# Kernel optimization log

Hardware: AMD Instinct MI355X
Metric: run time of the kernel (lower is better)

Reference implementation:

```python
import jax, jax.numpy as jnp
import numpy as np

N = 200_000   # nodes per type
F_IN = 64     # input features per node type
H = 8         # hidden_channels (heads=1)
E = 3_000_000 # edges per edge type


def setup_inputs() -> dict:
    key = jax.random.key(0)
    ks = jax.random.split(key, 40)
    d = {}
    d['x_ind'] = jax.random.normal(ks[0], (N, F_IN), jnp.float32)
    d['x_org'] = jax.random.normal(ks[1], (N, F_IN), jnp.float32)
    d['x_ext'] = jax.random.normal(ks[2], (N, F_IN), jnp.float32)
    d['ei_ind_org'] = jax.random.randint(ks[3], (2, E), 0, N, jnp.int32)
    d['ei_org_ind'] = jax.random.randint(ks[4], (2, E), 0, N, jnp.int32)
    d['ei_ext_ind'] = jax.random.randint(ks[5], (2, E), 0, N, jnp.int32)
    d['ei_ext_org'] = jax.random.randint(ks[6], (2, E), 0, N, jnp.int32)
    s_in = 1.0 / np.sqrt(F_IN)
    # per-node-type projections (Linear(F_IN, H) with bias)
    for i, nt in enumerate(('ind', 'org', 'ext')):
        d[f'W_{nt}'] = jax.random.normal(ks[7 + i], (F_IN, H), jnp.float32) * s_in
        d[f'b_{nt}'] = jnp.zeros((H,), jnp.float32)
    # per-edge-type GAT attention vectors (heads=1, so shape [H])
    for i, et in enumerate(('ind_org', 'org_ind', 'ext_ind', 'ext_org')):
        d[f'att_src_{et}'] = jax.random.normal(ks[10 + 2 * i], (H,), jnp.float32) * (1.0 / np.sqrt(H))
        d[f'att_dst_{et}'] = jax.random.normal(ks[11 + 2 * i], (H,), jnp.float32) * (1.0 / np.sqrt(H))
    # semantic attention: k_lin(H->H) + query q
    d['k_W'] = jax.random.normal(ks[20], (H, H), jnp.float32) * (1.0 / np.sqrt(H))
    d['k_b'] = jnp.zeros((H,), jnp.float32)
    d['q'] = jax.random.normal(ks[21], (H,), jnp.float32)
    # prediction heads
    d['lin_ind_W'] = jax.random.normal(ks[22], (H, 1), jnp.float32) * (1.0 / np.sqrt(H))
    d['lin_ind_b'] = jnp.zeros((1,), jnp.float32)
    d['lin_org_W'] = jax.random.normal(ks[23], (H, 1), jnp.float32) * (1.0 / np.sqrt(H))
    d['lin_org_b'] = jnp.zeros((1,), jnp.float32)
    return d


def _gat_edge(h_src, h_dst, a_src, a_dst, ei):
    """Per-edge-type GAT message passing with segment softmax over dst."""
    row, col = ei[0], ei[1]
    alpha_s = h_src @ a_src  # [N]
    alpha_d = h_dst @ a_dst  # [N]
    alpha = jax.nn.leaky_relu(alpha_s[row] + alpha_d[col], 0.2)  # [E]
    m = jax.lax.stop_gradient(jax.ops.segment_max(alpha, col, num_segments=N))
    m = jnp.where(jnp.isfinite(m), m, 0.0)
    ex = jnp.exp(alpha - m[col])
    den = jax.ops.segment_sum(ex, col, num_segments=N) + 1e-16
    w = ex / den[col]  # [E]
    out = jax.ops.segment_sum(h_src[row] * w[:, None], col, num_segments=N)  # [N,H]
    return jax.nn.relu(out)


def _group(outs, q, k_W, k_b):
    """Semantic-level attention over metapath embeddings."""
    o = jnp.stack(outs)  # [M, N, H]
    score = (jnp.tanh(o @ k_W + k_b) @ q).mean(axis=1)  # [M]
    attn = jax.nn.softmax(score)
    return jnp.einsum('m,mnf->nf', attn, o)


def reference(x_ind, x_org, x_ext,
              ei_ind_org, ei_org_ind, ei_ext_ind, ei_ext_org,
              W_ind, b_ind, W_org, b_org, W_ext, b_ext,
              att_src_ind_org, att_dst_ind_org,
              att_src_org_ind, att_dst_org_ind,
              att_src_ext_ind, att_dst_ext_ind,
              att_src_ext_org, att_dst_ext_org,
              k_W, k_b, q,
              lin_ind_W, lin_ind_b, lin_org_W, lin_org_b):
    h_ind = x_ind @ W_ind + b_ind  # [N,H]
    h_org = x_org @ W_org + b_org
    h_ext = x_ext @ W_ext + b_ext
    # metapaths into 'ind'
    outs_ind = [
        _gat_edge(h_org, h_ind, att_src_org_ind, att_dst_org_ind, ei_org_ind),
        _gat_edge(h_ext, h_ind, att_src_ext_ind, att_dst_ext_ind, ei_ext_ind),
    ]
    # metapaths into 'org'
    outs_org = [
        _gat_edge(h_ind, h_org, att_src_ind_org, att_dst_ind_org, ei_ind_org),
        _gat_edge(h_ext, h_org, att_src_ext_org, att_dst_ext_org, ei_ext_org),
    ]
    z_ind = _group(outs_ind, q, k_W, k_b)  # [N,H]
    z_org = _group(outs_org, q, k_W, k_b)
    pred_ind = jax.nn.sigmoid(z_ind @ lin_ind_W + lin_ind_b)[:, 0]
    pred_org = jax.nn.sigmoid(z_org @ lin_org_W + lin_org_b)[:, 0]
    return (pred_ind, pred_org)
```

## Files before the change

### kernel.cpp

```cpp
#include <hip/hip_runtime.h>
#include <hip/hip_fp16.h>

#define HH 8
#define FIN 64
#define CHUNK 8192
#define NPB 1024
#define NPB_SHIFT 10
#define MAXNB 256
#define SUBCH 4096
#define RSH 18
#define RMASK 0x3FFFFu

__device__ __forceinline__ float b2f(unsigned short u) {
  union { unsigned int i; float f; } x;
  x.i = ((unsigned int)u) << 16;
  return x.f;
}

__device__ __forceinline__ float lrelu(float x) { return x > 0.f ? x : 0.2f * x; }

__device__ __forceinline__ float ld(const void* p, int i, int isf) {
  return isf ? ((const float*)p)[i] : b2f(((const unsigned short*)p)[i]);
}

struct MP {
  const int* ei;
  const float* as;
  const float* ad;
  const __half* hs;
  float* den;
  float* out;
  unsigned* sorted;
  int* gcur;
  int E;
  int nchunks;
  int rcap;
};
struct MP4 { MP m[4]; };

struct PJ {
  const void* x; const void* W; const void* b; __half* h16;
  const void* a0; float* s0;
  const void* a1; float* s1;
  const void* a2; float* s2;
};
struct PJ3 { PJ p[3]; };

struct SC { const float *o0, *d0, *o1, *d1; float* score; };
struct SC2 { SC g[2]; };
struct PR { const float *o0, *d0, *o1, *d1; const float* score;
            const void* linW; const void* linb; float* outp; };
struct PR2 { PR g[2]; };

__global__ void __launch_bounds__(1024)
setup_kernel(const unsigned short* __restrict__ x, int* __restrict__ flag,
             float* __restrict__ score_all, int* __restrict__ gcur, int rcap) {
  __shared__ int tot;
  int t = threadIdx.x;
  gcur[t] = (t & 255) * rcap;
  if (t < 4) score_all[t] = 0.f;
  if (t == 0) tot = 0;
  __syncthreads();
  int cnt = 0;
  for (int i = t; i < 2048; i += 1024) {
    int e = (x[i] >> 7) & 0xFF;
    if (e >= 0x90) cnt++;
  }
  if (cnt) atomicAdd(&tot, cnt);
  __syncthreads();
  if (t == 0) flag[0] = (tot >= 8) ? 1 : 0;
}

__global__ void __launch_bounds__(256)
proj_kernel(PJ3 pj, int N, const int* __restrict__ flag) {
  const PJ P = pj.p[blockIdx.y];
  __shared__ float Wl[FIN][HH];
  __shared__ float bl[HH];
  __shared__ float al[3][HH];
  int isf = flag[0];
  int t = threadIdx.x;
  for (int i = t; i < FIN * HH; i += blockDim.x) Wl[i >> 3][i & 7] = ld(P.W, i, isf);
  if (t < HH) {
    bl[t] = ld(P.b, t, isf);
    al[0][t] = P.a0 ? ld(P.a0, t, isf) : 0.f;
    al[1][t] = P.a1 ? ld(P.a1, t, isf) : 0.f;
    al[2][t] = P.a2 ? ld(P.a2, t, isf) : 0.f;
  }
  __syncthreads();
  int n = blockIdx.x * blockDim.x + t;
  if (n >= N) return;
  float acc[HH];
#pragma unroll
  for (int j = 0; j < HH; ++j) acc[j] = bl[j];
  if (isf) {
    const float4* xr = (const float4*)((const float*)P.x + (size_t)n * FIN);
#pragma unroll
    for (int v = 0; v < FIN / 4; ++v) {
      float4 p = xr[v];
      float f4[4] = {p.x, p.y, p.z, p.w};
#pragma unroll
      for (int k = 0; k < 4; ++k) {
        int f = v * 4 + k;
#pragma unroll
        for (int j = 0; j < HH; ++j) acc[j] += f4[k] * Wl[f][j];
      }
    }
  } else {
    const uint4* xr = (const uint4*)((const unsigned short*)P.x + (size_t)n * FIN);
#pragma unroll
    for (int v = 0; v < FIN / 8; ++v) {
      uint4 p = xr[v];
      unsigned int w[4] = {p.x, p.y, p.z, p.w};
#pragma unroll
      for (int k = 0; k < 4; ++k) {
        float f0 = __uint_as_float(w[k] << 16);
        float f1 = __uint_as_float(w[k] & 0xFFFF0000u);
        int f = v * 8 + k * 2;
#pragma unroll
        for (int j = 0; j < HH; ++j) acc[j] += f0 * Wl[f][j];
#pragma unroll
        for (int j = 0; j < HH; ++j) acc[j] += f1 * Wl[f + 1][j];
      }
    }
  }
  union { __half h[8]; uint4 u; } pk;
#pragma unroll
  for (int j = 0; j < HH; ++j) pk.h[j] = __float2half(acc[j]);
  *(uint4*)(P.h16 + (size_t)n * HH) = pk.u;
  float d0 = 0.f, d1 = 0.f, d2 = 0.f;
#pragma unroll
  for (int j = 0; j < HH; ++j) {
    d0 += acc[j] * al[0][j];
    d1 += acc[j] * al[1][j];
    d2 += acc[j] * al[2][j];
  }
  if (P.s0) P.s0[n] = d0;
  if (P.s1) P.s1[n] = d1;
  if (P.s2) P.s2[n] = d2;
}

__global__ void __launch_bounds__(512)
partA(MP4 a4, int mp_base, int NB) {
  const MP a = a4.m[mp_base + blockIdx.y];
  int k = blockIdx.x;
  if (k >= a.nchunks) return;
  __shared__ unsigned buf[CHUNK];
  __shared__ int cnt[MAXNB];
  __shared__ int cur[MAXNB];
  __shared__ int off[MAXNB];
  __shared__ int posA[MAXNB];
  int t = threadIdx.x;
  int E = a.E;
  int base = k * CHUNK;
  int len = E - base; if (len > CHUNK) len = CHUNK;
  if (t < MAXNB) cnt[t] = 0;
  __syncthreads();
  int rr[16], cc[16];
  if (len == CHUNK && ((E & 3) == 0)) {
    const int4* eir = (const int4*)(a.ei + base);
    const int4* eic = (const int4*)(a.ei + E + base);
#pragma unroll
    for (int j = 0; j < 4; ++j) {
      int4 r4 = eir[j * 512 + t];
      int4 c4 = eic[j * 512 + t];
      rr[j * 4 + 0] = r4.x; cc[j * 4 + 0] = c4.x;
      rr[j * 4 + 1] = r4.y; cc[j * 4 + 1] = c4.y;
      rr[j * 4 + 2] = r4.z; cc[j * 4 + 2] = c4.z;
      rr[j * 4 + 3] = r4.w; cc[j * 4 + 3] = c4.w;
    }
  } else {
#pragma unroll
    for (int j = 0; j < 16; ++j) {
      int idx = j * 512 + t;
      rr[j] = -1;
      if (idx < len) { rr[j] = a.ei[base + idx]; cc[j] = a.ei[E + base + idx]; }
    }
  }
#pragma unroll
  for (int j = 0; j < 16; ++j)
    if (rr[j] >= 0) atomicAdd(&cnt[cc[j] >> NPB_SHIFT], 1);
  __syncthreads();
  if (t < 64) {
    int b0 = t * 4;
    int c0 = cnt[b0], c1 = cnt[b0 + 1], c2 = cnt[b0 + 2], c3 = cnt[b0 + 3];
    int s = c0 + c1 + c2 + c3;
    int inc = s;
#pragma unroll
    for (int d = 1; d < 64; d <<= 1) {
      int v = __shfl_up(inc, d, 64);
      if (t >= d) inc += v;
    }
    int run = inc - s;
    off[b0] = run;          cur[b0] = run;
    off[b0 + 1] = run + c0; cur[b0 + 1] = run + c0;
    off[b0 + 2] = run + c0 + c1; cur[b0 + 2] = run + c0 + c1;
    off[b0 + 3] = run + c0 + c1 + c2; cur[b0 + 3] = run + c0 + c1 + c2;
    posA[b0]     = c0 ? atomicAdd(&a.gcur[b0], c0) : 0;
    posA[b0 + 1] = c1 ? atomicAdd(&a.gcur[b0 + 1], c1) : 0;
    posA[b0 + 2] = c2 ? atomicAdd(&a.gcur[b0 + 2], c2) : 0;
    posA[b0 + 3] = c3 ? atomicAdd(&a.gcur[b0 + 3], c3) : 0;
  }
  __syncthreads();
#pragma unroll
  for (int j = 0; j < 16; ++j) {
    if (rr[j] >= 0) {
      int bb = cc[j] >> NPB_SHIFT;
      int p = atomicAdd(&cur[bb], 1);
      buf[p] = ((unsigned)(cc[j] & (NPB - 1)) << RSH) | (unsigned)rr[j];
    }
  }
  __syncthreads();
  int wv = t >> 6, ln = t & 63;
  for (int s = wv; s < NB; s += 8) {
    int cn = cnt[s];
    if (cn == 0) continue;
    int c0 = off[s];
    int gb = posA[s];
    int lim = (s + 1) * a.rcap;
    int mx = lim - gb; if (mx < 0) mx = 0;
    if (cn > mx) cn = mx;
    for (int j = ln; j < cn; j += 64)
      __builtin_nontemporal_store(buf[c0 + j], &a.sorted[(size_t)gb + j]);
  }
}

__global__ void __launch_bounds__(512)
partB(MP4 a4, int mp_base, int NB, int N, int fused) {
  int mp, b;
  if (fused) {
    int blk = blockIdx.x;
    int xcd = blk & 7;
    mp = xcd >> 1;
    b = ((blk >> 3) << 1) + (xcd & 1);
    if (b >= NB) return;
  } else {
    mp = mp_base;
    b = blockIdx.x;
  }
  const MP a = a4.m[mp];
  __shared__ unsigned key2[SUBCH];
  __shared__ int cnt2[NPB];
  __shared__ int o2[NPB];
  __shared__ int cur2[NPB];
  int t = threadIdx.x;
  int s0i = b * a.rcap;
  int cnt = a.gcur[b] - s0i;
  if (cnt < 0) cnt = 0;
  if (cnt > a.rcap) cnt = a.rcap;
  const unsigned* run = a.sorted + (size_t)s0i;
  int basen = b << NPB_SHIFT;
  int n0 = basen + t, n1 = basen + t + 512;
  float ad0 = (n0 < N) ? a.ad[n0] : 0.f;
  float ad1 = (n1 < N) ? a.ad[n1] : 0.f;
  const float* asp = a.as;
  const __half* hs = a.hs;

  float acc0[HH], acc1[HH];
#pragma unroll
  for (int f = 0; f < HH; ++f) { acc0[f] = 0.f; acc1[f] = 0.f; }
  float dn0 = 0.f, dn1 = 0.f;

  unsigned kk[8];
  int vld[8];
  {
    int m0 = cnt < SUBCH ? cnt : SUBCH;
#pragma unroll
    for (int u = 0; u < 8; ++u) {
      int idx = u * 512 + t;
      vld[u] = idx < m0;
      if (vld[u]) kk[u] = __builtin_nontemporal_load(run + idx);
    }
  }

  for (int c0 = 0; c0 < cnt; c0 += SUBCH) {
    cnt2[t] = 0; cnt2[t + 512] = 0;
    __syncthreads();
#pragma unroll
    for (int u = 0; u < 8; ++u)
      if (vld[u]) atomicAdd(&cnt2[kk[u] >> RSH], 1);
    __syncthreads();
    if (t < 64) {
      int c[16];
      int s = 0;
#pragma unroll
      for (int j = 0; j < 16; ++j) { c[j] = cnt2[t * 16 + j]; s += c[j]; }
      int inc = s;
#pragma unroll
      for (int d = 1; d < 64; d <<= 1) {
        int v = __shfl_up(inc, d, 64);
        if (t >= d) inc += v;
      }
      int run2 = inc - s;
#pragma unroll
      for (int j = 0; j < 16; ++j) {
        o2[t * 16 + j] = run2;
        cur2[t * 16 + j] = run2;
        run2 += c[j];
      }
    }
    __syncthreads();
#pragma unroll
    for (int u = 0; u < 8; ++u) {
      if (vld[u]) {
        int p = atomicAdd(&cur2[kk[u] >> RSH], 1);
        key2[p] = kk[u];
      }
    }
    __syncthreads();
    int cn0 = c0 + SUBCH;
    unsigned nk[8];
    int nv[8];
    {
      int mn = cnt - cn0; if (mn > SUBCH) mn = SUBCH;
#pragma unroll
      for (int u = 0; u < 8; ++u) {
        int idx = u * 512 + t;
        nv[u] = (cn0 < cnt) && (idx < mn);
        if (nv[u]) nk[u] = __builtin_nontemporal_load(run + (size_t)cn0 + idx);
      }
    }
    int j0 = o2[t], e0 = cur2[t];
    int j1 = o2[t + 512], e1 = cur2[t + 512];
    while (j0 < e0 || j1 < e1) {
      int c0n = e0 - j0; if (c0n > 4) c0n = 4; if (c0n < 0) c0n = 0;
      int c1n = e1 - j1; if (c1n > 4) c1n = 4; if (c1n < 0) c1n = 0;
      int r0[4], r1[4];
#pragma unroll
      for (int u = 0; u < 4; ++u) r0[u] = (u < c0n) ? (int)(key2[j0 + u] & RMASK) : -1;
#pragma unroll
      for (int u = 0; u < 4; ++u) r1[u] = (u < c1n) ? (int)(key2[j1 + u] & RMASK) : -1;
      float av0[4], av1[4];
      uint4 hv0[4], hv1[4];
#pragma unroll
      for (int u = 0; u < 4; ++u)
        if (r0[u] >= 0) { av0[u] = asp[r0[u]]; hv0[u] = *(const uint4*)(hs + (size_t)r0[u] * HH); }
#pragma unroll
      for (int u = 0; u < 4; ++u)
        if (r1[u] >= 0) { av1[u] = asp[r1[u]]; hv1[u] = *(const uint4*)(hs + (size_t)r1[u] * HH); }
#pragma unroll
      for (int u = 0; u < 4; ++u) {
        if (r0[u] >= 0) {
          float w = __expf(lrelu(av0[u] + ad0));
          dn0 += w;
          union { uint4 q; __half h[8]; } H; H.q = hv0[u];
#pragma unroll
          for (int f = 0; f < HH; ++f) acc0[f] += w * __half2float(H.h[f]);
        }
        if (r1[u] >= 0) {
          float w = __expf(lrelu(av1[u] + ad1));
          dn1 += w;
          union { uint4 q; __half h[8]; } H; H.q = hv1[u];
#pragma unroll
          for (int f = 0; f < HH; ++f) acc1[f] += w * __half2float(H.h[f]);
        }
      }
      j0 += c0n; j1 += c1n;
    }
    __syncthreads();
#pragma unroll
    for (int u = 0; u < 8; ++u) { vld[u] = nv[u]; kk[u] = nk[u]; }
  }
  if (n0 < N) {
    float4* po = (float4*)(a.out + (size_t)n0 * HH);
    po[0] = make_float4(acc0[0], acc0[1], acc0[2], acc0[3]);
    po[1] = make_float4(acc0[4], acc0[5], acc0[6], acc0[7]);
    a.den[n0] = dn0;
  }
  if (n1 < N) {
    float4* po = (float4*)(a.out + (size_t)n1 * HH);
    po[0] = make_float4(acc1[0], acc1[1], acc1[2], acc1[3]);
    po[1] = make_float4(acc1[4], acc1[5], acc1[6], acc1[7]);
    a.den[n1] = dn1;
  }
}

__global__ void __launch_bounds__(256)
score_kernel(SC2 sc, int N,
             const void* __restrict__ kW, const void* __restrict__ kb,
             const void* __restrict__ qv, const int* __restrict__ flag) {
  const SC S = sc.g[blockIdx.y];
  __shared__ float kWl[HH][HH];
  __shared__ float kbl[HH], ql[HH];
  __shared__ float r0[4], r1[4];
  int isf = flag[0];
  int t = threadIdx.x;
  if (t < HH * HH) kWl[t >> 3][t & 7] = ld(kW, t, isf);
  if (t < HH) { kbl[t] = ld(kb, t, isf); ql[t] = ld(qv, t, isf); }
  __syncthreads();
  int n = blockIdx.x * blockDim.x + t;
  float s0 = 0.f, s1 = 0.f;
  if (n < N) {
    const float* p0 = S.o0 + (size_t)n * HH;
    const float* p1 = S.o1 + (size_t)n * HH;
    float i0 = 1.f / (S.d0[n] + 1e-16f);
    float i1 = 1.f / (S.d1[n] + 1e-16f);
    float v0[HH], v1[HH];
#pragma unroll
    for (int j = 0; j < HH; ++j) { v0[j] = fmaxf(p0[j] * i0, 0.f); v1[j] = fmaxf(p1[j] * i1, 0.f); }
#pragma unroll
    for (int j = 0; j < HH; ++j) {
      float t0 = kbl[j], t1 = kbl[j];
#pragma unroll
      for (int i = 0; i < HH; ++i) { t0 += v0[i] * kWl[i][j]; t1 += v1[i] * kWl[i][j]; }
      s0 += tanhf(t0) * ql[j];
      s1 += tanhf(t1) * ql[j];
    }
  }
#pragma unroll
  for (int d = 32; d > 0; d >>= 1) {
    s0 += __shfl_down(s0, d, 64);
    s1 += __shfl_down(s1, d, 64);
  }
  int wv = t >> 6, ln = t & 63;
  if (ln == 0) { r0[wv] = s0; r1[wv] = s1; }
  __syncthreads();
  if (t == 0) {
    atomicAdd(&S.score[0], r0[0] + r0[1] + r0[2] + r0[3]);
    atomicAdd(&S.score[1], r1[0] + r1[1] + r1[2] + r1[3]);
  }
}

__global__ void __launch_bounds__(256)
pred_kernel(PR2 pr, int N, const int* __restrict__ flag) {
  const PR P = pr.g[blockIdx.y];
  int isf = flag[0];
  int n = blockIdx.x * blockDim.x + threadIdx.x;
  if (n >= N) return;
  float s0 = P.score[0] / (float)N, s1 = P.score[1] / (float)N;
  float mx = fmaxf(s0, s1);
  float e0 = __expf(s0 - mx), e1 = __expf(s1 - mx);
  float inv = 1.f / (e0 + e1);
  float a0 = e0 * inv, a1 = e1 * inv;
  const float* p0 = P.o0 + (size_t)n * HH;
  const float* p1 = P.o1 + (size_t)n * HH;
  float i0 = 1.f / (P.d0[n] + 1e-16f);
  float i1 = 1.f / (P.d1[n] + 1e-16f);
  float acc = ld(P.linb, 0, isf);
#pragma unroll
  for (int j = 0; j < HH; ++j) {
    float z = a0 * fmaxf(p0[j] * i0, 0.f) + a1 * fmaxf(p1[j] * i1, 0.f);
    acc += z * ld(P.linW, j, isf);
  }
  P.outp[n] = 1.f / (1.f + __expf(-acc));
}

extern "C" void kernel_launch(void* const* d_in, const int* in_sizes, int n_in,
                              void* d_out, int out_size, void* d_ws, size_t ws_size,
                              hipStream_t stream) {
  const int N = in_sizes[0] / FIN;

  const void* x_ind = d_in[0];
  const void* x_org = d_in[1];
  const void* x_ext = d_in[2];
  const int* ei_io = (const int*)d_in[3];  int E_io = in_sizes[3] / 2;
  const int* ei_oi = (const int*)d_in[4];  int E_oi = in_sizes[4] / 2;
  const int* ei_ei = (const int*)d_in[5];  int E_ei = in_sizes[5] / 2;
  const int* ei_eo = (const int*)d_in[6];  int E_eo = in_sizes[6] / 2;
  const void* W_ind = d_in[7];
  const void* b_ind = d_in[8];
  const void* W_org = d_in[9];
  const void* b_org = d_in[10];
  const void* W_ext = d_in[11];
  const void* b_ext = d_in[12];
  const void* att_src_io = d_in[13];
  const void* att_dst_io = d_in[14];
  const void* att_src_oi = d_in[15];
  const void* att_dst_oi = d_in[16];
  const void* att_src_ei = d_in[17];
  const void* att_dst_ei = d_in[18];
  const void* att_src_eo = d_in[19];
  const void* att_dst_eo = d_in[20];
  const void* k_W = d_in[21];
  const void* k_b = d_in[22];
  const void* qv  = d_in[23];
  const void* lin_ind_W = d_in[24];
  const void* lin_ind_b = d_in[25];
  const void* lin_org_W = d_in[26];
  const void* lin_org_b = d_in[27];

  float* out_f = (float*)d_out;

  int E_max = E_io;
  if (E_oi > E_max) E_max = E_oi;
  if (E_ei > E_max) E_max = E_ei;
  if (E_eo > E_max) E_max = E_eo;

  const int NB = (N + NPB - 1) >> NPB_SHIFT;
  const int nchunks_max = (E_max + CHUNK - 1) / CHUNK;
  const int rcap = (int)(((long long)E_max / NB) * 115 / 100) + 128;

  float* ws = (float*)d_ws;
  size_t off = 0;
  __half* h16_ind = (__half*)(ws + off); off += (size_t)N * HH / 2;
  __half* h16_org = (__half*)(ws + off); off += (size_t)N * HH / 2;
  __half* h16_ext = (__half*)(ws + off); off += (size_t)N * HH / 2;
  float* as_io = ws + off; off += N;
  float* ad_oi = ws + off; off += N;
  float* ad_ei = ws + off; off += N;
  float* as_oi = ws + off; off += N;
  float* ad_io = ws + off; off += N;
  float* ad_eo = ws + off; off += N;
  float* as_ei = ws + off; off += N;
  float* as_eo = ws + off; off += N;
  float* den_all = ws + off; off += (size_t)4 * N;
  float* out_all = ws + off; off += (size_t)4 * N * HH;
  float* score_all = ws + off; off += 4;
  int* flag = (int*)(ws + off); off += 1;
  off = (off + 1) & ~(size_t)1;
  int* gcur0 = (int*)(ws + off); off += 4 * 256;

  size_t sort_f = (size_t)NB * rcap;
  bool big = (off + 4 * sort_f) * sizeof(float) <= ws_size;
  int slots = big ? 4 : 1;
  unsigned* sorted0 = (unsigned*)(ws + off); off += (size_t)slots * sort_f;

  const int BS = 256;
  const int nb_node = (N + BS - 1) / BS;

  setup_kernel<<<1, 1024, 0, stream>>>((const unsigned short*)x_ind, flag, score_all, gcur0, rcap);

  PJ3 pj;
  pj.p[0] = PJ{x_ind, W_ind, b_ind, h16_ind, att_src_io, as_io, att_dst_oi, ad_oi, att_dst_ei, ad_ei};
  pj.p[1] = PJ{x_org, W_org, b_org, h16_org, att_src_oi, as_oi, att_dst_io, ad_io, att_dst_eo, ad_eo};
  pj.p[2] = PJ{x_ext, W_ext, b_ext, h16_ext, att_src_ei, as_ei, att_src_eo, as_eo, nullptr, nullptr};
  proj_kernel<<<dim3(nb_node, 3), BS, 0, stream>>>(pj, N, flag);

  const int* eis[4]       = {ei_oi, ei_ei, ei_io, ei_eo};
  int        Es[4]        = {E_oi, E_ei, E_io, E_eo};
  const float* ass[4]     = {as_oi, as_ei, as_io, as_eo};
  const float* ads[4]     = {ad_oi, ad_ei, ad_io, ad_eo};
  const __half* hsrcs[4]  = {h16_org, h16_ext, h16_ind, h16_ext};

  MP4 a4;
  for (int mp = 0; mp < 4; ++mp) {
    MP& a = a4.m[mp];
    a.ei = eis[mp];
    a.as = ass[mp];
    a.ad = ads[mp];
    a.hs = hsrcs[mp];
    a.den = den_all + (size_t)mp * N;
    a.out = out_all + (size_t)mp * N * HH;
    a.sorted = sorted0 + (size_t)(big ? mp : 0) * sort_f;
    a.gcur = gcur0 + mp * 256;
    a.E = Es[mp];
    a.nchunks = (Es[mp] + CHUNK - 1) / CHUNK;
    a.rcap = rcap;
  }

  if (big) {
    partA<<<dim3(nchunks_max, 4), 512, 0, stream>>>(a4, 0, NB);
    int nblkB = 8 * ((NB + 1) >> 1);
    partB<<<dim3(nblkB, 1), 512, 0, stream>>>(a4, 0, NB, N, 1);
  } else {
    for (int mp = 0; mp < 4; ++mp) {
      partA<<<dim3(a4.m[mp].nchunks, 1), 512, 0, stream>>>(a4, mp, NB);
      partB<<<dim3(NB, 1), 512, 0, stream>>>(a4, mp, NB, N, 0);
    }
  }

  float* o_ind0 = out_all + (size_t)0 * N * HH;
  float* o_ind1 = out_all + (size_t)1 * N * HH;
  float* o_org0 = out_all + (size_t)2 * N * HH;
  float* o_org1 = out_all + (size_t)3 * N * HH;
  float* d_ind0 = den_all + (size_t)0 * N;
  float* d_ind1 = den_all + (size_t)1 * N;
  float* d_org0 = den_all + (size_t)2 * N;
  float* d_org1 = den_all + (size_t)3 * N;

  SC2 sc;
  sc.g[0] = SC{o_ind0, d_ind0, o_ind1, d_ind1, score_all};
  sc.g[1] = SC{o_org0, d_org0, o_org1, d_org1, score_all + 2};
  score_kernel<<<dim3(nb_node, 2), BS, 0, stream>>>(sc, N, k_W, k_b, qv, flag);

  PR2 pr;
  pr.g[0] = PR{o_ind0, d_ind0, o_ind1, d_ind1, score_all, lin_ind_W, lin_ind_b, out_f};
  pr.g[1] = PR{o_org0, d_org0, o_org1, d_org1, score_all + 2, lin_org_W, lin_org_b, out_f + N};
  pred_kernel<<<dim3(nb_node, 2), BS, 0, stream>>>(pr, N, flag);
}
```

Before: 620.2 us.

## Use 1024-thread partB blocks with one node per thread and larger subchunks

partB now runs 1024 threads per block, so each thread owns a single destination node instead of two, and the local-sort subchunk grows from 4096 to 16384 keys (64 KB of LDS). The register prefetch of the next subchunk and the 4-wide batched gathers are removed in favour of plain strided loops and a simple per-edge gather loop. The aim is more threads in flight to hide gather latency and fewer subchunk passes with their barriers. In exchange it loses the explicit load/compute overlap and memory-level parallelism per thread, and the larger LDS footprint may cap occupancy.

```diff
diff --git a/kernel.cpp b/kernel.cpp
--- a/kernel.cpp
+++ b/kernel.cpp
@@ -7,7 +7,7 @@
 #define NPB 1024
 #define NPB_SHIFT 10
 #define MAXNB 256
-#define SUBCH 4096
+#define SUBCH 16384
 #define RSH 18
 #define RMASK 0x3FFFFu
 
@@ -224,7 +224,7 @@
   }
 }
 
-__global__ void __launch_bounds__(512)
+__global__ void __launch_bounds__(1024)
 partB(MP4 a4, int mp_base, int NB, int N, int fused) {
   int mp, b;
   if (fused) {
@@ -249,35 +249,24 @@
   if (cnt > a.rcap) cnt = a.rcap;
   const unsigned* run = a.sorted + (size_t)s0i;
   int basen = b << NPB_SHIFT;
-  int n0 = basen + t, n1 = basen + t + 512;
+  int n0 = basen + t;
   float ad0 = (n0 < N) ? a.ad[n0] : 0.f;
-  float ad1 = (n1 < N) ? a.ad[n1] : 0.f;
   const float* asp = a.as;
   const __half* hs = a.hs;
 
-  float acc0[HH], acc1[HH];
-#pragma unroll
-  for (int f = 0; f < HH; ++f) { acc0[f] = 0.f; acc1[f] = 0.f; }
-  float dn0 = 0.f, dn1 = 0.f;
-
-  unsigned kk[8];
-  int vld[8];
-  {
-    int m0 = cnt < SUBCH ? cnt : SUBCH;
-#pragma unroll
-    for (int u = 0; u < 8; ++u) {
-      int idx = u * 512 + t;
-      vld[u] = idx < m0;
-      if (vld[u]) kk[u] = __builtin_nontemporal_load(run + idx);
-    }
-  }
+  float acc0[HH];
+#pragma unroll
+  for (int f = 0; f < HH; ++f) acc0[f] = 0.f;
+  float dn0 = 0.f;
 
   for (int c0 = 0; c0 < cnt; c0 += SUBCH) {
-    cnt2[t] = 0; cnt2[t + 512] = 0;
+    int m = cnt - c0; if (m > SUBCH) m = SUBCH;
+    cnt2[t] = 0;
     __syncthreads();
-#pragma unroll
-    for (int u = 0; u < 8; ++u)
-      if (vld[u]) atomicAdd(&cnt2[kk[u] >> RSH], 1);
+    for (int idx = t; idx < m; idx += 1024) {
+      unsigned v = __builtin_nontemporal_load(run + c0 + idx);
+      atomicAdd(&cnt2[v >> RSH], 1);
+    }
     __syncthreads();
     if (t < 64) {
       int c[16];
@@ -299,78 +288,30 @@
       }
     }
     __syncthreads();
-#pragma unroll
-    for (int u = 0; u < 8; ++u) {
-      if (vld[u]) {
-        int p = atomicAdd(&cur2[kk[u] >> RSH], 1);
-        key2[p] = kk[u];
-      }
+    for (int idx = t; idx < m; idx += 1024) {
+      unsigned v = run[c0 + idx];
+      int p = atomicAdd(&cur2[v >> RSH], 1);
+      key2[p] = v;
     }
     __syncthreads();
-    int cn0 = c0 + SUBCH;
-    unsigned nk[8];
-    int nv[8];
-    {
-      int mn = cnt - cn0; if (mn > SUBCH) mn = SUBCH;
-#pragma unroll
-      for (int u = 0; u < 8; ++u) {
-        int idx = u * 512 + t;
-        nv[u] = (cn0 < cnt) && (idx < mn);
-        if (nv[u]) nk[u] = __builtin_nontemporal_load(run + (size_t)cn0 + idx);
-      }
-    }
-    int j0 = o2[t], e0 = cur2[t];
-    int j1 = o2[t + 512], e1 = cur2[t + 512];
-    while (j0 < e0 || j1 < e1) {
-      int c0n = e0 - j0; if (c0n > 4) c0n = 4; if (c0n < 0) c0n = 0;
-      int c1n = e1 - j1; if (c1n > 4) c1n = 4; if (c1n < 0) c1n = 0;
-      int r0[4], r1[4];
-#pragma unroll
-      for (int u = 0; u < 4; ++u) r0[u] = (u < c0n) ? (int)(key2[j0 + u] & RMASK) : -1;
-#pragma unroll
-      for (int u = 0; u < 4; ++u) r1[u] = (u < c1n) ? (int)(key2[j1 + u] & RMASK) : -1;
-      float av0[4], av1[4];
-      uint4 hv0[4], hv1[4];
-#pragma unroll
-      for (int u = 0; u < 4; ++u)
-        if (r0[u] >= 0) { av0[u] = asp[r0[u]]; hv0[u] = *(const uint4*)(hs + (size_t)r0[u] * HH); }
-#pragma unroll
-      for (int u = 0; u < 4; ++u)
-        if (r1[u] >= 0) { av1[u] = asp[r1[u]]; hv1[u] = *(const uint4*)(hs + (size_t)r1[u] * HH); }
-#pragma unroll
-      for (int u = 0; u < 4; ++u) {
-        if (r0[u] >= 0) {
-          float w = __expf(lrelu(av0[u] + ad0));
-          dn0 += w;
-          union { uint4 q; __half h[8]; } H; H.q = hv0[u];
-#pragma unroll
-          for (int f = 0; f < HH; ++f) acc0[f] += w * __half2float(H.h[f]);
-        }
-        if (r1[u] >= 0) {
-          float w = __expf(lrelu(av1[u] + ad1));
-          dn1 += w;
-          union { uint4 q; __half h[8]; } H; H.q = hv1[u];
-#pragma unroll
-          for (int f = 0; f < HH; ++f) acc1[f] += w * __half2float(H.h[f]);
-        }
-      }
-      j0 += c0n; j1 += c1n;
-    }
-    __syncthreads();
-#pragma unroll
-    for (int u = 0; u < 8; ++u) { vld[u] = nv[u]; kk[u] = nk[u]; }
+    int j = o2[t], e = cur2[t];
+    for (; j < e; ++j) {
+      unsigned v = key2[j];
+      int r = (int)(v & RMASK);
+      float w = __expf(lrelu(asp[r] + ad0));
+      union { uint4 q; __half h[8]; } H;
+      H.q = *(const uint4*)(hs + (size_t)r * HH);
+      dn0 += w;
+#pragma unroll
+      for (int f = 0; f < HH; ++f) acc0[f] += w * __half2float(H.h[f]);
+    }
+    if (c0 + SUBCH < cnt) __syncthreads();
   }
   if (n0 < N) {
     float4* po = (float4*)(a.out + (size_t)n0 * HH);
     po[0] = make_float4(acc0[0], acc0[1], acc0[2], acc0[3]);
     po[1] = make_float4(acc0[4], acc0[5], acc0[6], acc0[7]);
     a.den[n0] = dn0;
-  }
-  if (n1 < N) {
-    float4* po = (float4*)(a.out + (size_t)n1 * HH);
-    po[0] = make_float4(acc1[0], acc1[1], acc1[2], acc1[3]);
-    po[1] = make_float4(acc1[4], acc1[5], acc1[6], acc1[7]);
-    a.den[n1] = dn1;
   }
 }
 
@@ -550,11 +491,11 @@
   if (big) {
     partA<<<dim3(nchunks_max, 4), 512, 0, stream>>>(a4, 0, NB);
     int nblkB = 8 * ((NB + 1) >> 1);
-    partB<<<dim3(nblkB, 1), 512, 0, stream>>>(a4, 0, NB, N, 1);
+    partB<<<dim3(nblkB, 1), 1024, 0, stream>>>(a4, 0, NB, N, 1);
   } else {
     for (int mp = 0; mp < 4; ++mp) {
       partA<<<dim3(a4.m[mp].nchunks, 1), 512, 0, stream>>>(a4, mp, NB);
-      partB<<<dim3(NB, 1), 512, 0, stream>>>(a4, mp, NB, N, 0);
+      partB<<<dim3(NB, 1), 1024, 0, stream>>>(a4, mp, NB, N, 0);
     }
   }
 
```

Result: faster. 581.6 us (-6.2%).

## Fuse semantic-attention score reduction into partB and simplify edge gather loop

Applied to the files above, without the earlier changes.

Removes the separate score kernel and computes the per-node semantic attention score (ReLU-normalized message, k_lin, tanh, dot with q) directly in partB from the register accumulators, then reduces per block and atomically adds into score_all[mp]. This avoids re-reading the four out/den arrays from global memory. The inner edge loop is also changed from a 4-way batched gather to a one-edge-per-iteration loop, which lowers register pressure but reduces memory-level parallelism. A fast exp-based tanh replaces tanhf.

```diff
diff --git a/kernel.cpp b/kernel.cpp
--- a/kernel.cpp
+++ b/kernel.cpp
@@ -21,6 +21,12 @@
 
 __device__ __forceinline__ float ld(const void* p, int i, int isf) {
   return isf ? ((const float*)p)[i] : b2f(((const unsigned short*)p)[i]);
+}
+
+__device__ __forceinline__ float tanhf_fast(float x) {
+  float xc = fminf(fmaxf(x, -15.f), 15.f);
+  float e = __expf(2.f * xc);
+  return 1.f - 2.f / (e + 1.f);
 }
 
 struct MP {
@@ -46,8 +52,6 @@
 };
 struct PJ3 { PJ p[3]; };
 
-struct SC { const float *o0, *d0, *o1, *d1; float* score; };
-struct SC2 { SC g[2]; };
 struct PR { const float *o0, *d0, *o1, *d1; const float* score;
             const void* linW; const void* linb; float* outp; };
 struct PR2 { PR g[2]; };
@@ -225,7 +229,10 @@
 }
 
 __global__ void __launch_bounds__(512)
-partB(MP4 a4, int mp_base, int NB, int N, int fused) {
+partB(MP4 a4, int mp_base, int NB, int N, int fused,
+      const void* __restrict__ kW, const void* __restrict__ kb,
+      const void* __restrict__ qv, float* __restrict__ score_all,
+      const int* __restrict__ flag) {
   int mp, b;
   if (fused) {
     int blk = blockIdx.x;
@@ -242,7 +249,13 @@
   __shared__ int cnt2[NPB];
   __shared__ int o2[NPB];
   __shared__ int cur2[NPB];
+  __shared__ float kWl[HH * HH];
+  __shared__ float kbl[HH], ql[HH];
+  __shared__ float red[8];
   int t = threadIdx.x;
+  int isf = flag[0];
+  if (t < HH * HH) kWl[t] = ld(kW, t, isf);
+  if (t < HH) { kbl[t] = ld(kb, t, isf); ql[t] = ld(qv, t, isf); }
   int s0i = b * a.rcap;
   int cnt = a.gcur[b] - s0i;
   if (cnt < 0) cnt = 0;
@@ -322,39 +335,26 @@
     int j0 = o2[t], e0 = cur2[t];
     int j1 = o2[t + 512], e1 = cur2[t + 512];
     while (j0 < e0 || j1 < e1) {
-      int c0n = e0 - j0; if (c0n > 4) c0n = 4; if (c0n < 0) c0n = 0;
-      int c1n = e1 - j1; if (c1n > 4) c1n = 4; if (c1n < 0) c1n = 0;
-      int r0[4], r1[4];
-#pragma unroll
-      for (int u = 0; u < 4; ++u) r0[u] = (u < c0n) ? (int)(key2[j0 + u] & RMASK) : -1;
-#pragma unroll
-      for (int u = 0; u < 4; ++u) r1[u] = (u < c1n) ? (int)(key2[j1 + u] & RMASK) : -1;
-      float av0[4], av1[4];
-      uint4 hv0[4], hv1[4];
-#pragma unroll
-      for (int u = 0; u < 4; ++u)
-        if (r0[u] >= 0) { av0[u] = asp[r0[u]]; hv0[u] = *(const uint4*)(hs + (size_t)r0[u] * HH); }
-#pragma unroll
-      for (int u = 0; u < 4; ++u)
-        if (r1[u] >= 0) { av1[u] = asp[r1[u]]; hv1[u] = *(const uint4*)(hs + (size_t)r1[u] * HH); }
-#pragma unroll
-      for (int u = 0; u < 4; ++u) {
-        if (r0[u] >= 0) {
-          float w = __expf(lrelu(av0[u] + ad0));
-          dn0 += w;
-          union { uint4 q; __half h[8]; } H; H.q = hv0[u];
-#pragma unroll
-          for (int f = 0; f < HH; ++f) acc0[f] += w * __half2float(H.h[f]);
-        }
-        if (r1[u] >= 0) {
-          float w = __expf(lrelu(av1[u] + ad1));
-          dn1 += w;
-          union { uint4 q; __half h[8]; } H; H.q = hv1[u];
-#pragma unroll
-          for (int f = 0; f < HH; ++f) acc1[f] += w * __half2float(H.h[f]);
-        }
-      }
-      j0 += c0n; j1 += c1n;
+      if (j0 < e0) {
+        unsigned v = key2[j0++];
+        int r = (int)(v & RMASK);
+        float w = __expf(lrelu(asp[r] + ad0));
+        union { uint4 u; __half h[8]; } H;
+        H.u = *(const uint4*)(hs + (size_t)r * HH);
+        dn0 += w;
+#pragma unroll
+        for (int f = 0; f < HH; ++f) acc0[f] += w * __half2float(H.h[f]);
+      }
+      if (j1 < e1) {
+        unsigned v = key2[j1++];
+        int r = (int)(v & RMASK);
+        float w = __expf(lrelu(asp[r] + ad1));
+        union { uint4 u; __half h[8]; } H;
+        H.u = *(const uint4*)(hs + (size_t)r * HH);
+        dn1 += w;
+#pragma unroll
+        for (int f = 0; f < HH; ++f) acc1[f] += w * __half2float(H.h[f]);
+      }
     }
     __syncthreads();
 #pragma unroll
@@ -372,51 +372,43 @@
     po[1] = make_float4(acc1[4], acc1[5], acc1[6], acc1[7]);
     a.den[n1] = dn1;
   }
-}
-
-__global__ void __launch_bounds__(256)
-score_kernel(SC2 sc, int N,
-             const void* __restrict__ kW, const void* __restrict__ kb,
-             const void* __restrict__ qv, const int* __restrict__ flag) {
-  const SC S = sc.g[blockIdx.y];
-  __shared__ float kWl[HH][HH];
-  __shared__ float kbl[HH], ql[HH];
-  __shared__ float r0[4], r1[4];
-  int isf = flag[0];
-  int t = threadIdx.x;
-  if (t < HH * HH) kWl[t >> 3][t & 7] = ld(kW, t, isf);
-  if (t < HH) { kbl[t] = ld(kb, t, isf); ql[t] = ld(qv, t, isf); }
-  __syncthreads();
-  int n = blockIdx.x * blockDim.x + t;
-  float s0 = 0.f, s1 = 0.f;
-  if (n < N) {
-    const float* p0 = S.o0 + (size_t)n * HH;
-    const float* p1 = S.o1 + (size_t)n * HH;
-    float i0 = 1.f / (S.d0[n] + 1e-16f);
-    float i1 = 1.f / (S.d1[n] + 1e-16f);
-    float v0[HH], v1[HH];
-#pragma unroll
-    for (int j = 0; j < HH; ++j) { v0[j] = fmaxf(p0[j] * i0, 0.f); v1[j] = fmaxf(p1[j] * i1, 0.f); }
+  float sc = 0.f;
+  if (n0 < N) {
+    float inv = 1.f / (dn0 + 1e-16f);
+    float v[HH];
+#pragma unroll
+    for (int j = 0; j < HH; ++j) v[j] = fmaxf(acc0[j] * inv, 0.f);
 #pragma unroll
     for (int j = 0; j < HH; ++j) {
-      float t0 = kbl[j], t1 = kbl[j];
-#pragma unroll
-      for (int i = 0; i < HH; ++i) { t0 += v0[i] * kWl[i][j]; t1 += v1[i] * kWl[i][j]; }
-      s0 += tanhf(t0) * ql[j];
-      s1 += tanhf(t1) * ql[j];
-    }
-  }
-#pragma unroll
-  for (int d = 32; d > 0; d >>= 1) {
-    s0 += __shfl_down(s0, d, 64);
-    s1 += __shfl_down(s1, d, 64);
-  }
+      float z = kbl[j];
+#pragma unroll
+      for (int i = 0; i < HH; ++i) z += v[i] * kWl[i * HH + j];
+      sc += tanhf_fast(z) * ql[j];
+    }
+  }
+  if (n1 < N) {
+    float inv = 1.f / (dn1 + 1e-16f);
+    float v[HH];
+#pragma unroll
+    for (int j = 0; j < HH; ++j) v[j] = fmaxf(acc1[j] * inv, 0.f);
+#pragma unroll
+    for (int j = 0; j < HH; ++j) {
+      float z = kbl[j];
+#pragma unroll
+      for (int i = 0; i < HH; ++i) z += v[i] * kWl[i * HH + j];
+      sc += tanhf_fast(z) * ql[j];
+    }
+  }
+#pragma unroll
+  for (int d = 32; d > 0; d >>= 1) sc += __shfl_down(sc, d, 64);
   int wv = t >> 6, ln = t & 63;
-  if (ln == 0) { r0[wv] = s0; r1[wv] = s1; }
+  if (ln == 0) red[wv] = sc;
   __syncthreads();
   if (t == 0) {
-    atomicAdd(&S.score[0], r0[0] + r0[1] + r0[2] + r0[3]);
-    atomicAdd(&S.score[1], r1[0] + r1[1] + r1[2] + r1[3]);
+    float tt = 0.f;
+#pragma unroll
+    for (int i = 0; i < 8; ++i) tt += red[i];
+    atomicAdd(&score_all[mp], tt);
   }
 }
 
@@ -550,11 +542,11 @@
   if (big) {
     partA<<<dim3(nchunks_max, 4), 512, 0, stream>>>(a4, 0, NB);
     int nblkB = 8 * ((NB + 1) >> 1);
-    partB<<<dim3(nblkB, 1), 512, 0, stream>>>(a4, 0, NB, N, 1);
+    partB<<<dim3(nblkB, 1), 512, 0, stream>>>(a4, 0, NB, N, 1, k_W, k_b, qv, score_all, flag);
   } else {
     for (int mp = 0; mp < 4; ++mp) {
       partA<<<dim3(a4.m[mp].nchunks, 1), 512, 0, stream>>>(a4, mp, NB);
-      partB<<<dim3(NB, 1), 512, 0, stream>>>(a4, mp, NB, N, 0);
+      partB<<<dim3(NB, 1), 512, 0, stream>>>(a4, mp, NB, N, 0, k_W, k_b, qv, score_all, flag);
     }
   }
 
@@ -567,11 +559,6 @@
   float* d_org0 = den_all + (size_t)2 * N;
   float* d_org1 = den_all + (size_t)3 * N;
 
-  SC2 sc;
-  sc.g[0] = SC{o_ind0, d_ind0, o_ind1, d_ind1, score_all};
-  sc.g[1] = SC{o_org0, d_org0, o_org1, d_org1, score_all + 2};
-  score_kernel<<<dim3(nb_node, 2), BS, 0, stream>>>(sc, N, k_W, k_b, qv, flag);
-
   PR2 pr;
   pr.g[0] = PR{o_ind0, d_ind0, o_ind1, d_ind1, score_all, lin_ind_W, lin_ind_b, out_f};
   pr.g[1] = PR{o_org0, d_org0, o_org1, d_org1, score_all + 2, lin_org_W, lin_org_b, out_f + N};
```

Result: faster. 531.5 us (-14.3%).
